# Kernel optimization log

Hardware: AMD Instinct MI355X
Metric: run time of the kernel (lower is better)

## Reference

```python
import jax, jax.numpy as jnp
import numpy as np

B, T, C, H, HD = 4, 2048, 1024, 16, 64

def setup_inputs() -> dict:
    key = jax.random.key(0)
    ks = jax.random.split(key, 9)
    s = 1.0 / np.sqrt(C)
    return {
        "x":  jax.random.normal(ks[0], (B, T, C), jnp.float32),
        "Wq": jax.random.normal(ks[1], (H, C, HD), jnp.float32) * s,
        "bq": jax.random.normal(ks[2], (H, HD), jnp.float32) * 0.02,
        "Wk": jax.random.normal(ks[3], (H, C, HD), jnp.float32) * s,
        "bk": jax.random.normal(ks[4], (H, HD), jnp.float32) * 0.02,
        "Wv": jax.random.normal(ks[5], (H, C, HD), jnp.float32) * s,
        "bv": jax.random.normal(ks[6], (H, HD), jnp.float32) * 0.02,
        "Wo": jax.random.normal(ks[7], (C, C), jnp.float32) * s,
        "bo": jax.random.normal(ks[8], (C,), jnp.float32) * 0.02,
    }

def reference(x, Wq, bq, Wk, bk, Wv, bv, Wo, bo):
    # Batched per-head linear projections: [B,T,C] x [H,C,D] -> [B,H,T,D]
    q = jnp.einsum('btc,hcd->bhtd', x, Wq) + bq[None, :, None, :]
    k = jnp.einsum('btc,hcd->bhtd', x, Wk) + bk[None, :, None, :]
    v = jnp.einsum('btc,hcd->bhtd', x, Wv) + bv[None, :, None, :]
    scale = 1.0 / jnp.sqrt(jnp.asarray(HD, q.dtype))
    scores = jnp.einsum('bhtd,bhsd->bhts', q, k) * scale  # [B,H,T,T]
    causal = jnp.tril(jnp.ones((T, T), dtype=bool))
    scores = jnp.where(causal[None, None, :, :], scores, -jnp.inf)
    attn = jax.nn.softmax(scores, axis=-1)
    out = jnp.einsum('bhts,bhsd->bhtd', attn, v)          # [B,H,T,D]
    concat = out.transpose(0, 2, 1, 3).reshape(B, T, C)   # concat heads
    return concat @ Wo + bo
```

## Files before the change

### kernel.cpp

```cpp
#include <hip/hip_runtime.h>
#include <stdint.h>

#define TSEQ 2048
#define NHEAD 16

typedef __attribute__((ext_vector_type(8))) short bf16x8;
typedef __attribute__((ext_vector_type(4))) short bf16x4;
typedef __attribute__((ext_vector_type(4))) float f32x4;

__device__ __forceinline__ unsigned short f2bf(float f) {
  union { float f; uint32_t u; } c;
  c.f = f;
  uint32_t u = c.u;
  u += 0x7fffu + ((u >> 16) & 1u);
  return (unsigned short)(u >> 16);
}

using as3_void  = __attribute__((address_space(3))) void;
using as1_cvoid = const __attribute__((address_space(1))) void;

__device__ __forceinline__ void gld_lds16(const void* g, void* l) {
  __builtin_amdgcn_global_load_lds((as1_cvoid*)g, (as3_void*)l, 16, 0, 0);
}


__global__ void cast_x_kernel(const float4* __restrict__ x, unsigned short* __restrict__ xb) {
  int i = blockIdx.x * 256 + threadIdx.x;
  float4 v = x[i];
  int e = i * 4;
  int m = e >> 10, k = e & 1023;
  int ks = k ^ ((m & 7) << 3);
  ushort4 o;
  o.x = f2bf(v.x); o.y = f2bf(v.y); o.z = f2bf(v.z); o.w = f2bf(v.w);
  *(ushort4*)(xb + (size_t)m * 1024 + ks) = o;
}

__global__ void repack_wqkv(const float* __restrict__ Wq, const float* __restrict__ Wk,
                            const float* __restrict__ Wv, unsigned short* __restrict__ BT) {
  __shared__ unsigned short tile[64][72];
  const float* W = (blockIdx.z == 0) ? Wq : (blockIdx.z == 1) ? Wk : Wv;
  const int h = blockIdx.y;
  const int c0 = blockIdx.x * 64;
  const int t = threadIdx.x;
  const float* src = W + ((size_t)h * 1024 + c0) * 64;
#pragma unroll
  for (int p = 0; p < 16; ++p) {
    int idx = p * 256 + t;
    int cc = idx >> 6, d = idx & 63;
    tile[cc][d] = f2bf(src[(size_t)cc * 64 + d]);
  }
  __syncthreads();
  unsigned short* dst = BT + ((size_t)blockIdx.z * 1024 + (size_t)h * 64) * 1024 + c0;
#pragma unroll
  for (int p = 0; p < 16; ++p) {
    int idx = p * 256 + t;
    int d = idx >> 6, cc = idx & 63;
    dst[(size_t)d * 1024 + (cc ^ ((d & 7) << 3))] = tile[cc][d];
  }
}

__global__ void repack_wo(const float* __restrict__ Wo, unsigned short* __restrict__ WoT) {
  __shared__ unsigned short tile[64][72];
  const int k0 = blockIdx.x * 64;
  const int n0 = blockIdx.y * 64;
  const int t = threadIdx.x;
#pragma unroll
  for (int p = 0; p < 16; ++p) {
    int idx = p * 256 + t;
    int kk = idx >> 6, nn = idx & 63;
    tile[kk][nn] = f2bf(Wo[(size_t)(k0 + kk) * 1024 + n0 + nn]);
  }
  __syncthreads();
#pragma unroll
  for (int p = 0; p < 16; ++p) {
    int idx = p * 256 + t;
    int nn = idx >> 6, kk = idx & 63;
    WoT[(size_t)(n0 + nn) * 1024 + k0 + (kk ^ ((nn & 7) << 3))] = tile[kk][nn];
  }
}


template <int MODE>
__global__ __launch_bounds__(256) void gemm_bt(
    const unsigned short* __restrict__ A, const unsigned short* __restrict__ BTm,
    const float* __restrict__ bias0, const float* __restrict__ bias1,
    const float* __restrict__ bias2,
    unsigned short* __restrict__ qo, unsigned short* __restrict__ ko,
    unsigned short* __restrict__ vto, float* __restrict__ outf,
    int K, int N) {
  __shared__ __align__(16) char lds[(MODE == 1) ? 36864 : 32768];
  unsigned short* As = (unsigned short*)lds;
  unsigned short* Bs = (unsigned short*)(lds + 16384);

  const int tid = threadIdx.x, lane = tid & 63, wv = tid >> 6;
  const int wr = wv >> 1, wc = wv & 1;
  const int g = lane >> 4, r = lane & 15;
  const int m0 = blockIdx.x * 128, n0 = blockIdx.y * 128;
  const int xr = (r & 7) << 4;

  f32x4 acc[4][4] = {};

  const int arow = tid >> 3;
  const int acol = (tid & 7) * 8;
  const unsigned short* Ab = A + (size_t)(m0 + arow) * K + acol;
  const unsigned short* Bb = BTm + (size_t)(n0 + arow) * K + acol;
  char* AsB = (char*)As + wv * 1024;
  char* BsB = (char*)Bs + wv * 1024;

  for (int k0 = 0; k0 < K; k0 += 64) {
#pragma unroll
    for (int i = 0; i < 4; ++i) {
      gld_lds16(Ab + (size_t)i * 32 * K + k0, AsB + i * 4096);
      gld_lds16(Bb + (size_t)i * 32 * K + k0, BsB + i * 4096);
    }
    __syncthreads();
    const char* Ar = (const char*)As;
    const char* Br = (const char*)Bs;
#pragma unroll
    for (int kk = 0; kk < 2; ++kk) {
      bf16x8 af[4], bfv[4];
#pragma unroll
      for (int f = 0; f < 4; ++f) {
        af[f]  = *(const bf16x8*)(Ar + (wr * 64 + f * 16 + r) * 128 + ((kk * 64 + g * 16) ^ xr));
        bfv[f] = *(const bf16x8*)(Br + (wc * 64 + f * 16 + r) * 128 + ((kk * 64 + g * 16) ^ xr));
      }
#pragma unroll
      for (int fm = 0; fm < 4; ++fm)
#pragma unroll
        for (int fn = 0; fn < 4; ++fn)
          acc[fm][fn] = __builtin_amdgcn_mfma_f32_16x16x32_bf16(af[fm], bfv[fn], acc[fm][fn], 0, 0, 0);
    }
    __syncthreads();
  }

  if (MODE == 0) {
    const int which = n0 >> 10;
    const float* bias = (which == 0) ? bias0 : (which == 1) ? bias1 : bias2;
    const int b = m0 >> 11;
    const int t0 = m0 & 2047;
    unsigned short* ep = (unsigned short*)lds;

#pragma unroll
    for (int h = 0; h < 2; ++h) {
      const int head = ((n0 & 1023) + h * 64) >> 6;
      const size_t bhb = (size_t)(b * NHEAD + head) * 131072;
      __syncthreads();
      if (wc == h) {
        if (which == 2) {
#pragma unroll
          for (int fn = 0; fn < 4; ++fn) {
            const int d = fn * 16 + r;
            const float bvl = bias[head * 64 + d];
#pragma unroll
            for (int fm = 0; fm < 4; ++fm)
#pragma unroll
              for (int j = 0; j < 4; ++j) {
                const int t = wr * 64 + fm * 16 + 4 * g + j;
                ep[d * 136 + t] = f2bf(acc[fm][fn][j] + bvl);
              }
          }
        } else {
#pragma unroll
          for (int fn = 0; fn < 4; ++fn) {
            const int d = fn * 16 + r;
            const float bvl = bias[head * 64 + d];
#pragma unroll
            for (int fm = 0; fm < 4; ++fm)
#pragma unroll
              for (int j = 0; j < 4; ++j) {
                const int t = wr * 64 + fm * 16 + 4 * g + j;
                ep[t * 72 + d] = f2bf(acc[fm][fn][j] + bvl);
              }
          }
        }
      }
      __syncthreads();
      if (which == 2) {
#pragma unroll
        for (int p = 0; p < 4; ++p) {
          const int d = p * 16 + (tid >> 4);
          const int u = tid & 15;
          const int c = u >> 3;
          const int w = u & 7;
          const int kk = w >> 2, gg = w & 3;
          const int base_t = c * 64 + kk * 32 + 4 * gg;
          union { bf16x4 h4[2]; bf16x8 v8; } cc2;
          cc2.h4[0] = *(const bf16x4*)(ep + d * 136 + base_t);
          cc2.h4[1] = *(const bf16x4*)(ep + d * 136 + base_t + 16);
          const int q_base = w * 8;
          *(bf16x8*)(vto + bhb + (size_t)((t0 >> 6) + c) * 4096 + (size_t)d * 64 +
                     (q_base ^ ((d & 7) << 3))) = cc2.v8;
        }
      } else {
        unsigned short* qk = (which == 1) ? ko : qo;
#pragma unroll
        for (int p = 0; p < 4; ++p) {
          const int row = p * 32 + (tid >> 3);
          const int seg = tid & 7;
          const bf16x8 v8 = *(const bf16x8*)(ep + row * 72 + seg * 8);
          const int tt = t0 + row;
          int dbase = seg * 8;
          if (which == 1) dbase ^= (tt & 7) << 3;
          *(bf16x8*)(qk + bhb + (size_t)tt * 64 + dbase) = v8;
        }
      }
    }
  } else {
    float* epf = (float*)lds;
#pragma unroll
    for (int h = 0; h < 2; ++h) {
      __syncthreads();
      if (wc == h) {
#pragma unroll
        for (int fn = 0; fn < 4; ++fn) {
          const int n = n0 + h * 64 + fn * 16 + r;
          const float bvl = bias0[n];
#pragma unroll
          for (int fm = 0; fm < 4; ++fm)
#pragma unroll
            for (int j = 0; j < 4; ++j)
              epf[(wr * 64 + fm * 16 + 4 * g + j) * 68 + fn * 16 + r] = acc[fm][fn][j] + bvl;
        }
      }
      __syncthreads();
#pragma unroll
      for (int p = 0; p < 8; ++p) {
        const int row = p * 16 + (tid >> 4);
        const int seg = tid & 15;
        const f32x4 v4 = *(const f32x4*)(epf + row * 68 + seg * 4);
        *(f32x4*)(outf + (size_t)(m0 + row) * N + n0 + h * 64 + seg * 4) = v4;
      }
    }
  }
}


__global__ __launch_bounds__(256) void attn_fwd(const unsigned short* __restrict__ Qm,
                                                const unsigned short* __restrict__ Km,
                                                const unsigned short* __restrict__ Vtm,
                                                unsigned short* __restrict__ Om) {
  __shared__ __align__(16) unsigned short Ks[2][4096];
  __shared__ __align__(16) unsigned short Vs[2][4096];

  const int tid = threadIdx.x, lane = tid & 63, wv = tid >> 6;
  const int g = lane >> 4, r = lane & 15;
  const int bh = blockIdx.x & 63;
  const int qp = 15 - (blockIdx.x >> 6);

  const unsigned short* Qp = Qm + (size_t)bh * 131072;
  const unsigned short* Kp = Km + (size_t)bh * 131072;
  const unsigned short* Vp = Vtm + (size_t)bh * 131072;

  const int qb[2] = {qp * 128 + wv * 16, qp * 128 + 64 + wv * 16};

  bf16x8 qf[2][2];
#pragma unroll
  for (int mi = 0; mi < 2; ++mi)
#pragma unroll
    for (int h2 = 0; h2 < 2; ++h2)
      qf[mi][h2] = *(const bf16x8*)(Qp + (size_t)(qb[mi] + r) * 64 + h2 * 32 + g * 8);

  f32x4 oacc[2][4] = {};
  float m_[2] = {-__builtin_inff(), -__builtin_inff()};
  float l_[2] = {0.f, 0.f};

#define ASTAGE(buf, c) do {                                                      \
    const unsigned short* kg_ = Kp + (size_t)(c) * 4096;                         \
    const unsigned short* vg_ = Vp + (size_t)(c) * 4096;                         \
    const int o0_ = wv * 1024;                                                   \
    gld_lds16(kg_ + (o0_ >> 1) + lane * 8, (char*)Ks[buf] + o0_);                \
    gld_lds16(vg_ + (o0_ >> 1) + lane * 8, (char*)Vs[buf] + o0_);                \
    gld_lds16(kg_ + ((o0_ + 4096) >> 1) + lane * 8, (char*)Ks[buf] + o0_ + 4096);\
    gld_lds16(vg_ + ((o0_ + 4096) >> 1) + lane * 8, (char*)Vs[buf] + o0_ + 4096);\
  } while (0)

  const int nt = qp * 2 + 2;
  ASTAGE(0, 0);
  __syncthreads();

  for (int t = 0; t < nt; ++t) {
    const int cur = t & 1;
    if (t + 1 < nt) ASTAGE(cur ^ 1, t + 1);

    const char* KsT = (const char*)Ks[cur];
    const char* VsT = (const char*)Vs[cur];
    const int sw = (r & 7) << 4;
    bf16x8 kf[4][2], vf[4][2];
#pragma unroll
    for (int tt = 0; tt < 4; ++tt) {
      const int rowb = (tt * 16 + r) * 128;
#pragma unroll
      for (int kk = 0; kk < 2; ++kk) {
        const int cb = (kk * 64 + g * 16) ^ sw;
        kf[tt][kk] = *(const bf16x8*)(KsT + rowb + cb);
        vf[tt][kk] = *(const bf16x8*)(VsT + rowb + cb);
      }
    }

#pragma unroll
    for (int mi = 0; mi < 2; ++mi) {
      const int qbm = qb[mi];
      if (t * 64 > qbm + 15) continue;

      f32x4 sT[4];
      __builtin_amdgcn_s_setprio(1);
#pragma unroll
      for (int tt = 0; tt < 4; ++tt) {
        f32x4 a = {0.f, 0.f, 0.f, 0.f};
        a = __builtin_amdgcn_mfma_f32_16x16x32_bf16(kf[tt][0], qf[mi][0], a, 0, 0, 0);
        a = __builtin_amdgcn_mfma_f32_16x16x32_bf16(kf[tt][1], qf[mi][1], a, 0, 0, 0);
        sT[tt] = a;
      }
      __builtin_amdgcn_s_setprio(0);

      const int qg = qbm + r;
      float mx = -__builtin_inff();
      if (t * 64 + 63 > qbm) {
#pragma unroll
        for (int tt = 0; tt < 4; ++tt)
#pragma unroll
          for (int j = 0; j < 4; ++j) {
            const int kv = t * 64 + tt * 16 + 4 * g + j;
            float sv = sT[tt][j] * 0.125f;
            sv = (kv <= qg) ? sv : -__builtin_inff();
            sT[tt][j] = sv;
            mx = fmaxf(mx, sv);
          }
      } else {
#pragma unroll
        for (int tt = 0; tt < 4; ++tt)
#pragma unroll
          for (int j = 0; j < 4; ++j) {
            const float sv = sT[tt][j] * 0.125f;
            sT[tt][j] = sv;
            mx = fmaxf(mx, sv);
          }
      }
      mx = fmaxf(mx, __shfl_xor(mx, 16));
      mx = fmaxf(mx, __shfl_xor(mx, 32));

      float mcur = m_[mi];
      const bool norescale = __all(mx <= mcur + 4.0f);
      float rs = 1.f;
      if (!norescale) {
        const float mnew = fmaxf(mcur, mx);
        rs = __expf(mcur - mnew);
        m_[mi] = mnew;
        mcur = mnew;
      }
      float ts = 0.f;
#pragma unroll
      for (int tt = 0; tt < 4; ++tt)
#pragma unroll
        for (int j = 0; j < 4; ++j) {
          const float p = __expf(sT[tt][j] - mcur);
          sT[tt][j] = p;
          ts += p;
        }
      ts += __shfl_xor(ts, 16);
      ts += __shfl_xor(ts, 32);
      if (!norescale) {
        l_[mi] = l_[mi] * rs + ts;
        float rsb[4];
#pragma unroll
        for (int j = 0; j < 4; ++j) rsb[j] = __shfl(rs, 4 * g + j);
#pragma unroll
        for (int df = 0; df < 4; ++df)
#pragma unroll
          for (int j = 0; j < 4; ++j) oacc[mi][df][j] *= rsb[j];
      } else {
        l_[mi] += ts;
      }

      union { uint32_t w[8]; bf16x8 v[2]; } pu;
#pragma unroll
      for (int tt = 0; tt < 4; ++tt) {
        asm("v_cvt_pk_bf16_f32 %0, %1, %2" : "=v"(pu.w[2 * tt])
            : "v"(sT[tt][0]), "v"(sT[tt][1]));
        asm("v_cvt_pk_bf16_f32 %0, %1, %2" : "=v"(pu.w[2 * tt + 1])
            : "v"(sT[tt][2]), "v"(sT[tt][3]));
      }

      __builtin_amdgcn_s_setprio(1);
#pragma unroll
      for (int kk = 0; kk < 2; ++kk)
#pragma unroll
        for (int df = 0; df < 4; ++df)
          oacc[mi][df] = __builtin_amdgcn_mfma_f32_16x16x32_bf16(pu.v[kk], vf[df][kk], oacc[mi][df], 0, 0, 0);
      __builtin_amdgcn_s_setprio(0);
    }
    __syncthreads();
  }
#undef ASTAGE

  const int b = bh >> 4, h = bh & 15;
#pragma unroll
  for (int mi = 0; mi < 2; ++mi) {
    float lb[4];
#pragma unroll
    for (int j = 0; j < 4; ++j) lb[j] = __shfl(l_[mi], 4 * g + j);
#pragma unroll
    for (int df = 0; df < 4; ++df)
#pragma unroll
      for (int j = 0; j < 4; ++j) {
        const int trow = qb[mi] + 4 * g + j;
        const float ov = oacc[mi][df][j] / lb[j];
        const int col = (df * 16 + r) ^ ((trow & 7) << 3);
        Om[((size_t)(b * TSEQ + trow)) * 1024 + h * 64 + col] = f2bf(ov);
      }
  }
}


extern "C" void kernel_launch(void* const* d_in, const int* in_sizes, int n_in,
                              void* d_out, int out_size, void* d_ws, size_t ws_size,
                              hipStream_t stream) {
  const float* x  = (const float*)d_in[0];
  const float* Wq = (const float*)d_in[1];
  const float* bq = (const float*)d_in[2];
  const float* Wk = (const float*)d_in[3];
  const float* bk = (const float*)d_in[4];
  const float* Wv = (const float*)d_in[5];
  const float* bv = (const float*)d_in[6];
  const float* Wo = (const float*)d_in[7];
  const float* bo = (const float*)d_in[8];
  float* out = (float*)d_out;

  unsigned short* xb  = (unsigned short*)d_ws;
  unsigned short* btq = xb + (size_t)8192 * 1024;
  unsigned short* wot = btq + (size_t)3072 * 1024;
  unsigned short* qb  = wot + (size_t)1024 * 1024;
  unsigned short* kb  = qb + (size_t)64 * 2048 * 64;
  unsigned short* vtb = kb + (size_t)64 * 2048 * 64;

  cast_x_kernel<<<8192, 256, 0, stream>>>((const float4*)x, xb);
  repack_wqkv<<<dim3(16, 16, 3), 256, 0, stream>>>(Wq, Wk, Wv, btq);
  repack_wo<<<dim3(16, 16), 256, 0, stream>>>(Wo, wot);

  gemm_bt<0><<<dim3(64, 24), 256, 0, stream>>>(xb, btq, bq, bk, bv, qb, kb, vtb,
                                               nullptr, 1024, 3072);
  attn_fwd<<<1024, 256, 0, stream>>>(qb, kb, vtb, xb);
  gemm_bt<1><<<dim3(64, 8), 256, 0, stream>>>(xb, wot, bo, nullptr, nullptr,
                                              nullptr, nullptr, nullptr, out,
                                              1024, 1024);
}
```

Before: 197.5 us.

## Fold softmax scale and log2e into Q projection, use exp2 and deferred row sums

The Q projection epilogue now multiplies by scale*log2(e), so the attention loop drops its per-score multiply and uses the hardware exp2 directly. Cross-lane shuffles for the row max happen only when a rescale is needed. The per-lane partial row sums are reduced once at the end instead of every tile. The final divide becomes a reciprocal multiply. This trims VALU and shuffle work in the softmax inner loop, in exchange for slightly different rounding (Q scaled before bf16 quantization, approximate rcp) and a rescale check that now compares per-lane maxima against the running max.

Measured after the change: 181.8 us. 7.9% less time.

```diff
diff --git a/kernel.cpp b/kernel.cpp
--- a/kernel.cpp
+++ b/kernel.cpp
@@ -14,6 +14,14 @@
   uint32_t u = c.u;
   u += 0x7fffu + ((u >> 16) & 1u);
   return (unsigned short)(u >> 16);
+}
+
+__device__ __forceinline__ float fexp2(float x) {
+#if __has_builtin(__builtin_amdgcn_exp2f)
+  return __builtin_amdgcn_exp2f(x);
+#else
+  return __builtin_exp2f(x);
+#endif
 }
 
 using as3_void  = __attribute__((address_space(3))) void;
@@ -136,6 +144,7 @@
   if (MODE == 0) {
     const int which = n0 >> 10;
     const float* bias = (which == 0) ? bias0 : (which == 1) ? bias1 : bias2;
+    const float sc = (which == 0) ? 0.18033688011112042f : 1.0f;
     const int b = m0 >> 11;
     const int t0 = m0 & 2047;
     unsigned short* ep = (unsigned short*)lds;
@@ -169,7 +178,7 @@
 #pragma unroll
               for (int j = 0; j < 4; ++j) {
                 const int t = wr * 64 + fm * 16 + 4 * g + j;
-                ep[t * 72 + d] = f2bf(acc[fm][fn][j] + bvl);
+                ep[t * 72 + d] = f2bf((acc[fm][fn][j] + bvl) * sc);
               }
           }
         }
@@ -314,63 +323,52 @@
       __builtin_amdgcn_s_setprio(0);
 
       const int qg = qbm + r;
-      float mx = -__builtin_inff();
       if (t * 64 + 63 > qbm) {
 #pragma unroll
         for (int tt = 0; tt < 4; ++tt)
 #pragma unroll
           for (int j = 0; j < 4; ++j) {
             const int kv = t * 64 + tt * 16 + 4 * g + j;
-            float sv = sT[tt][j] * 0.125f;
-            sv = (kv <= qg) ? sv : -__builtin_inff();
-            sT[tt][j] = sv;
-            mx = fmaxf(mx, sv);
+            sT[tt][j] = (kv <= qg) ? sT[tt][j] : -__builtin_inff();
           }
-      } else {
-#pragma unroll
-        for (int tt = 0; tt < 4; ++tt)
-#pragma unroll
-          for (int j = 0; j < 4; ++j) {
-            const float sv = sT[tt][j] * 0.125f;
-            sT[tt][j] = sv;
-            mx = fmaxf(mx, sv);
-          }
-      }
-      mx = fmaxf(mx, __shfl_xor(mx, 16));
-      mx = fmaxf(mx, __shfl_xor(mx, 32));
+      }
+
+      float tm[4];
+#pragma unroll
+      for (int tt = 0; tt < 4; ++tt)
+        tm[tt] = fmaxf(fmaxf(sT[tt][0], sT[tt][1]), fmaxf(sT[tt][2], sT[tt][3]));
+      const float mx = fmaxf(fmaxf(tm[0], tm[1]), fmaxf(tm[2], tm[3]));
 
       float mcur = m_[mi];
       const bool norescale = __all(mx <= mcur + 4.0f);
-      float rs = 1.f;
       if (!norescale) {
-        const float mnew = fmaxf(mcur, mx);
-        rs = __expf(mcur - mnew);
+        float rmx = mx;
+        rmx = fmaxf(rmx, __shfl_xor(rmx, 16));
+        rmx = fmaxf(rmx, __shfl_xor(rmx, 32));
+        const float mnew = fmaxf(mcur, rmx);
+        const float rs = fexp2(mcur - mnew);
         m_[mi] = mnew;
         mcur = mnew;
-      }
+        l_[mi] *= rs;
+        float rsb[4];
+#pragma unroll
+        for (int j = 0; j < 4; ++j) rsb[j] = __shfl(rs, 4 * g + j);
+#pragma unroll
+        for (int df = 0; df < 4; ++df)
+#pragma unroll
+          for (int j = 0; j < 4; ++j) oacc[mi][df][j] *= rsb[j];
+      }
+
       float ts = 0.f;
 #pragma unroll
       for (int tt = 0; tt < 4; ++tt)
 #pragma unroll
         for (int j = 0; j < 4; ++j) {
-          const float p = __expf(sT[tt][j] - mcur);
+          const float p = fexp2(sT[tt][j] - mcur);
           sT[tt][j] = p;
           ts += p;
         }
-      ts += __shfl_xor(ts, 16);
-      ts += __shfl_xor(ts, 32);
-      if (!norescale) {
-        l_[mi] = l_[mi] * rs + ts;
-        float rsb[4];
-#pragma unroll
-        for (int j = 0; j < 4; ++j) rsb[j] = __shfl(rs, 4 * g + j);
-#pragma unroll
-        for (int df = 0; df < 4; ++df)
-#pragma unroll
-          for (int j = 0; j < 4; ++j) oacc[mi][df][j] *= rsb[j];
-      } else {
-        l_[mi] += ts;
-      }
+      l_[mi] += ts;
 
       union { uint32_t w[8]; bf16x8 v[2]; } pu;
 #pragma unroll
@@ -396,15 +394,21 @@
   const int b = bh >> 4, h = bh & 15;
 #pragma unroll
   for (int mi = 0; mi < 2; ++mi) {
-    float lb[4];
-#pragma unroll
-    for (int j = 0; j < 4; ++j) lb[j] = __shfl(l_[mi], 4 * g + j);
+    float lt = l_[mi];
+    lt += __shfl_xor(lt, 16);
+    lt += __shfl_xor(lt, 32);
+    float inv[4];
+#pragma unroll
+    for (int j = 0; j < 4; ++j) {
+      const float lb = __shfl(lt, 4 * g + j);
+      inv[j] = __builtin_amdgcn_rcpf(lb);
+    }
 #pragma unroll
     for (int df = 0; df < 4; ++df)
 #pragma unroll
       for (int j = 0; j < 4; ++j) {
         const int trow = qb[mi] + 4 * g + j;
-        const float ov = oacc[mi][df][j] / lb[j];
+        const float ov = oacc[mi][df][j] * inv[j];
         const int col = (df * 16 + r) ^ ((trow & 7) << 3);
         Om[((size_t)(b * TSEQ + trow)) * 1024 + h * 64 + col] = f2bf(ov);
       }
```
